# Optimization experiments

Measured on AMD Instinct MI355X. Metric: run time of the kernel, lower is better.

Reference implementation:

```python
import jax, jax.numpy as jnp
import numpy as np

NX, NY, NZ = 432, 496, 1
VX, VY, VZ = 0.16, 0.16, 4.0
XOFF = VX / 2 + 0.0
YOFF = VY / 2 + (-39.68)
ZOFF = VZ / 2 + (-3.0)
GRID = NZ * NX * NY
P, NPT, B = 100000, 32, 8
EPS = 1e-3


def setup_inputs() -> dict:
    key = jax.random.key(0)
    k1, k2, k3, k4 = jax.random.split(key, 4)
    voxels = jax.random.normal(k1, (P, NPT, 4), dtype=jnp.float32)
    num_points = jax.random.randint(k2, (P,), 1, NPT + 1, dtype=jnp.int32)
    b = jax.random.randint(k3, (P,), 0, B, dtype=jnp.int32)
    # unique BEV cells (17 coprime with GRID, P < GRID) -> deterministic scatter
    cell = (jnp.arange(P, dtype=jnp.int32) * 17) % GRID
    y = cell // NX
    x = cell % NX
    coords = jnp.stack([b, jnp.zeros_like(b), y, x], axis=1)  # [P,4] (b,z,y,x)
    W = jax.random.normal(k4, (64, 10), dtype=jnp.float32) * 0.1
    gamma = jnp.ones((64,), dtype=jnp.float32)
    beta = jnp.zeros((64,), dtype=jnp.float32)
    return {"voxels": voxels, "num_points": num_points, "coords": coords,
            "W": W, "gamma": gamma, "beta": beta}


def reference(voxels, num_points, coords, W, gamma, beta):
    cf = coords.astype(voxels.dtype)
    npf = num_points.astype(voxels.dtype)
    # cluster feature: offset from pillar mean
    points_mean = voxels[:, :, :3].sum(axis=1, keepdims=True) / npf[:, None, None]
    f_cluster = voxels[:, :, :3] - points_mean
    # center feature: offset from voxel center
    cx = cf[:, 3, None] * VX + XOFF
    cy = cf[:, 2, None] * VY + YOFF
    cz = cf[:, 1, None] * VZ + ZOFF
    f_center = jnp.stack([voxels[:, :, 0] - cx,
                          voxels[:, :, 1] - cy,
                          voxels[:, :, 2] - cz], axis=-1)
    feat = jnp.concatenate([voxels, f_cluster, f_center], axis=-1)  # [P,N,10]
    mask = (jnp.arange(NPT, dtype=jnp.int32)[None, :] < num_points[:, None])
    feat = feat * mask.astype(feat.dtype)[:, :, None]
    # linear(10->64, no bias) + BatchNorm1d (batch stats, biased var) + relu
    x = jnp.einsum('pnf,cf->pnc', feat, W)  # [P,N,64]
    mean = x.mean(axis=(0, 1))
    var = ((x - mean) ** 2).mean(axis=(0, 1))
    x = (x - mean) * jax.lax.rsqrt(var + EPS) * gamma + beta
    x = jax.nn.relu(x)
    pillars = x.max(axis=1)  # [P,64]
    idx = coords[:, 1] + coords[:, 2] * NX + coords[:, 3]
    bev = jnp.zeros((B, GRID, 64), dtype=pillars.dtype)
    bev = bev.at[coords[:, 0], idx].set(pillars)
    bev = jnp.transpose(bev, (0, 2, 1))  # [B,64,GRID]
    return bev.reshape(B, 64 * NZ, NY, NX)
```

## Files before the change

kernel.cpp:

```cpp
#include <hip/hip_runtime.h>

typedef unsigned short u16;

#define NXg 432
#define NYg 496
#define GRIDg (NXg*NYg)
#define NPTg 32
#define Bg 8
#define CHg 64
#define NSLOT 32

__device__ __forceinline__ float bf2f(u16 u){
    union { unsigned int i; float f; } x; x.i = ((unsigned int)u) << 16; return x.f;
}
__device__ __forceinline__ u16 f2bf(float f){
    union { float f; unsigned int i; } x; x.f = f;
    unsigned int i = x.i + 0x7FFFu + ((x.i >> 16) & 1u);
    return (u16)(i >> 16);
}
__device__ __forceinline__ bool is_bf16(const void* gamma){
    return ((*(const unsigned*)gamma) & 0xFFFFu) != 0u;
}

__global__ __launch_bounds__(256) void pfe_init(int* __restrict__ map, float* __restrict__ chsum,
                                                u16* __restrict__ pv, int P){
    int t = blockIdx.x*256 + threadIdx.x;
    ((int4*)map)[t] = make_int4(-1,-1,-1,-1);
    if (t < (NSLOT*128)/4) ((float4*)chsum)[t] = make_float4(0.f,0.f,0.f,0.f);
    if (t < 8) ((uint4*)(pv + (size_t)P*CHg))[t] = make_uint4(0u,0u,0u,0u);
}

__global__ __launch_bounds__(256) void pfe_pillar(
    const void* __restrict__ vox, const int* __restrict__ nump,
    const int* __restrict__ coords, const void* __restrict__ Wv,
    const void* __restrict__ gv,
    u16* __restrict__ pv, int* __restrict__ map, float* __restrict__ chsum,
    int P, int nwaves)
{
    __shared__ float4 pts[4][32];
    const bool isbf = is_bf16(gv);
    int lane = threadIdx.x & 63;
    int wid  = (blockIdx.x*256 + threadIdx.x) >> 6;
    int ws   = threadIdx.x >> 6;
    int n    = lane & 31;

    float w4,w5,w6,w7,w8,w9, wp0,wp1,wp2,wp3;
    bool gsel;
    {
        float w[10];
#pragma unroll
        for (int j=0;j<10;j++)
            w[j] = isbf ? bf2f(((const u16*)Wv)[lane*10 + j]) : ((const float*)Wv)[lane*10 + j];
        wp0 = w[0]+w[4]+w[7];
        wp1 = w[1]+w[5]+w[8];
        wp2 = w[2]+w[6]+w[9];
        wp3 = w[3];
        w4=w[4]; w5=w[5]; w6=w[6]; w7=w[7]; w8=w[8]; w9=w[9];
        float g = isbf ? bf2f(((const u16*)gv)[lane]) : ((const float*)gv)[lane];
        gsel = (g >= 0.f);
    }

    float sx = 0.f, sx2 = 0.f;

    for (int p = wid; p < P; p += nwaves) {
        int np = nump[p];
        int4 cc = *(const int4*)(coords + 4*p);
        float4 pt;
        if (isbf){
            ushort4 raw = *(const ushort4*)((const u16*)vox + ((size_t)p*NPTg + n)*4);
            pt = make_float4(bf2f(raw.x), bf2f(raw.y), bf2f(raw.z), bf2f(raw.w));
        } else {
            pt = *(const float4*)((const float*)vox + ((size_t)p*NPTg + n)*4);
        }
        if (lane < 32) pts[ws][n] = pt;

        float s0 = pt.x, s1 = pt.y, s2 = pt.z;
#pragma unroll
        for (int m = 1; m < 32; m <<= 1){
            s0 += __shfl_xor(s0, m, 64);
            s1 += __shfl_xor(s1, m, 64);
            s2 += __shfl_xor(s2, m, 64);
        }
        float inv = 1.0f / (float)np;
        float m0 = s0*inv, m1 = s1*inv, m2 = s2*inv;
        float ccx = (float)cc.w * 0.16f + 0.08f;
        float ccy = (float)cc.z * 0.16f + (0.08f - 39.68f);
        float ccz = (float)cc.y * 4.0f  + (2.0f - 3.0f);
        float d = -(m0*w4 + m1*w5 + m2*w6 + ccx*w7 + ccy*w8 + ccz*w9);

        const float4* row = pts[ws];
        float qmx = -3e38f, qmn = 3e38f, sq = 0.f, sq2 = 0.f;
        int k = 0;
        for (; k + 4 <= np; k += 4){
#pragma unroll
            for (int u = 0; u < 4; u++){
                float4 a = row[k+u];
                float q = fmaf(a.x, wp0, fmaf(a.y, wp1, fmaf(a.z, wp2, a.w*wp3)));
                qmx = fmaxf(qmx, q);
                qmn = fminf(qmn, q);
                sq += q;
                sq2 = fmaf(q, q, sq2);
            }
        }
        for (; k < np; k++){
            float4 a = row[k];
            float q = fmaf(a.x, wp0, fmaf(a.y, wp1, fmaf(a.z, wp2, a.w*wp3)));
            qmx = fmaxf(qmx, q);
            qmn = fminf(qmn, q);
            sq += q;
            sq2 = fmaf(q, q, sq2);
        }

        float npf = (float)np;
        sx  += sq + npf*d;
        sx2 += sq2 + d*(2.f*sq + npf*d);

        float fmx = qmx + d, fmn = qmn + d;
        if (np < NPTg){ fmx = fmaxf(fmx, 0.f); fmn = fminf(fmn, 0.f); }
        pv[(size_t)p*CHg + lane] = f2bf(gsel ? fmx : fmn);
        if (lane == 0) map[cc.x*GRIDg + cc.z*NXg + cc.w] = p;
    }

    float* slot = chsum + (blockIdx.x & (NSLOT-1))*128;
    atomicAdd(slot + lane, sx);
    atomicAdd(slot + 64 + lane, sx2);
}

__global__ __launch_bounds__(64) void pfe_stats(
    const float* __restrict__ chsum,
    const void* __restrict__ gv, const void* __restrict__ bv,
    float* __restrict__ sb, int P)
{
    const bool isbf = is_bf16(gv);
    int t = threadIdx.x;
    float S = 0.f, S2 = 0.f;
    for (int sl = 0; sl < NSLOT; sl++){
        S  += chsum[sl*128 + t];
        S2 += chsum[sl*128 + 64 + t];
    }
    float cnt = (float)P * (float)NPTg;
    float mean = S / cnt;
    float var  = S2 / cnt - mean*mean;
    float g  = isbf ? bf2f(((const u16*)gv)[t]) : ((const float*)gv)[t];
    float be = isbf ? bf2f(((const u16*)bv)[t]) : ((const float*)bv)[t];
    float sc = g * rsqrtf(var + 1e-3f);
    sb[t] = sc; sb[64 + t] = be - mean*sc;
}

__global__ __launch_bounds__(256) void pfe_postbn(
    u16* __restrict__ pv, const float* __restrict__ sb,
    const void* __restrict__ gv, int P)
{
    if (!is_bf16(gv)) return;
    int t = blockIdx.x*256 + threadIdx.x;
    if (t >= P*8) return;
    size_t i0 = (size_t)t*8;
    int c0 = (int)(i0 & 63);
    uint4 v = *(uint4*)(pv + i0);
    float4 sA = *(const float4*)(sb + c0);
    float4 sB = *(const float4*)(sb + c0 + 4);
    float4 bA = *(const float4*)(sb + 64 + c0);
    float4 bB = *(const float4*)(sb + 64 + c0 + 4);
#define PB(dw, slo, blo, shi, bhi) \
    ( (unsigned)f2bf(fmaxf(fmaf(slo, bf2f((u16)((dw) & 0xFFFFu)), blo), 0.f)) \
    | ((unsigned)f2bf(fmaxf(fmaf(shi, bf2f((u16)((dw) >> 16)),    bhi), 0.f)) << 16) )
    unsigned o0 = PB(v.x, sA.x, bA.x, sA.y, bA.y);
    unsigned o1 = PB(v.y, sA.z, bA.z, sA.w, bA.w);
    unsigned o2 = PB(v.z, sB.x, bB.x, sB.y, bB.y);
    unsigned o3 = PB(v.w, sB.z, bB.z, sB.w, bB.w);
#undef PB
    *(uint4*)(pv + i0) = make_uint4(o0, o1, o2, o3);
}

__global__ __launch_bounds__(192) void pfe_gather(
    const int* __restrict__ map, const u16* __restrict__ pv,
    const float* __restrict__ sb, const void* __restrict__ gv,
    void* __restrict__ out, int P)
{
    const bool isbf = is_bf16(gv);
    int b  = blockIdx.z;
    int c0 = blockIdx.y * 32;
    int px = blockIdx.x*768 + threadIdx.x*4;
    int4 m4 = *(const int4*)(map + (size_t)b*GRIDg + px);

    if (isbf){
        int p0 = (m4.x < 0) ? P : m4.x;
        int p1 = (m4.y < 0) ? P : m4.y;
        int p2 = (m4.z < 0) ? P : m4.z;
        int p3 = (m4.w < 0) ? P : m4.w;
        const uint4* r0 = (const uint4*)(pv + (size_t)p0*CHg + c0);
        const uint4* r1 = (const uint4*)(pv + (size_t)p1*CHg + c0);
        const uint4* r2 = (const uint4*)(pv + (size_t)p2*CHg + c0);
        const uint4* r3 = (const uint4*)(pv + (size_t)p3*CHg + c0);
        uint4 A0=r0[0], A1=r0[1], A2=r0[2], A3=r0[3];
        uint4 B0=r1[0], B1=r1[1], B2=r1[2], B3=r1[3];
        uint4 C0=r2[0], C1=r2[1], C2=r2[2], C3=r2[3];
        uint4 D0=r3[0], D1=r3[1], D2=r3[2], D3=r3[3];
        u16* ob = (u16*)out + ((size_t)(b*CHg + c0))*GRIDg + px;
#define GETB(Q0,Q1,Q2,Q3, COMP, CREL) { \
        unsigned w0=Q0.COMP, w1=Q1.COMP, w2=Q2.COMP, w3=Q3.COMP; \
        uint2 e, o; \
        e.x = __builtin_amdgcn_perm(w1, w0, 0x05040100u); \
        e.y = __builtin_amdgcn_perm(w3, w2, 0x05040100u); \
        o.x = __builtin_amdgcn_perm(w1, w0, 0x07060302u); \
        o.y = __builtin_amdgcn_perm(w3, w2, 0x07060302u); \
        *(uint2*)(ob + (size_t)(CREL)*GRIDg)     = e; \
        *(uint2*)(ob + (size_t)((CREL)+1)*GRIDg) = o; }
        GETB(A0,B0,C0,D0, x, 0)  GETB(A0,B0,C0,D0, y, 2)  GETB(A0,B0,C0,D0, z, 4)  GETB(A0,B0,C0,D0, w, 6)
        GETB(A1,B1,C1,D1, x, 8)  GETB(A1,B1,C1,D1, y, 10) GETB(A1,B1,C1,D1, z, 12) GETB(A1,B1,C1,D1, w, 14)
        GETB(A2,B2,C2,D2, x, 16) GETB(A2,B2,C2,D2, y, 18) GETB(A2,B2,C2,D2, z, 20) GETB(A2,B2,C2,D2, w, 22)
        GETB(A3,B3,C3,D3, x, 24) GETB(A3,B3,C3,D3, y, 26) GETB(A3,B3,C3,D3, z, 28) GETB(A3,B3,C3,D3, w, 30)
#undef GETB
    } else {
        bool v0 = m4.x >= 0, v1 = m4.y >= 0, v2 = m4.z >= 0, v3 = m4.w >= 0;
        int p0 = v0 ? m4.x : 0;
        int p1 = v1 ? m4.y : 0;
        int p2 = v2 ? m4.z : 0;
        int p3 = v3 ? m4.w : 0;
        const uint4* r0 = (const uint4*)(pv + (size_t)p0*CHg + c0);
        const uint4* r1 = (const uint4*)(pv + (size_t)p1*CHg + c0);
        const uint4* r2 = (const uint4*)(pv + (size_t)p2*CHg + c0);
        const uint4* r3 = (const uint4*)(pv + (size_t)p3*CHg + c0);
        uint4 A0=r0[0], A1=r0[1], A2=r0[2], A3=r0[3];
        uint4 B0=r1[0], B1=r1[1], B2=r1[2], B3=r1[3];
        uint4 C0=r2[0], C1=r2[1], C2=r2[2], C3=r2[3];
        uint4 D0=r3[0], D1=r3[1], D2=r3[2], D3=r3[3];
        float* obf = (float*)out + ((size_t)(b*CHg + c0))*GRIDg + px;
#define GETF(Q0,Q1,Q2,Q3, COMP, CREL) { \
        unsigned w0=Q0.COMP, w1=Q1.COMP, w2=Q2.COMP, w3=Q3.COMP; \
        float sce = sb[c0+(CREL)],   bie = sb[64+c0+(CREL)]; \
        float sco = sb[c0+(CREL)+1], bio = sb[64+c0+(CREL)+1]; \
        float4 oe, oo; \
        oe.x = v0 ? fmaxf(fmaf(sce, __uint_as_float(w0 << 16), bie), 0.f) : 0.f; \
        oe.y = v1 ? fmaxf(fmaf(sce, __uint_as_float(w1 << 16), bie), 0.f) : 0.f; \
        oe.z = v2 ? fmaxf(fmaf(sce, __uint_as_float(w2 << 16), bie), 0.f) : 0.f; \
        oe.w = v3 ? fmaxf(fmaf(sce, __uint_as_float(w3 << 16), bie), 0.f) : 0.f; \
        oo.x = v0 ? fmaxf(fmaf(sco, __uint_as_float(w0 & 0xFFFF0000u), bio), 0.f) : 0.f; \
        oo.y = v1 ? fmaxf(fmaf(sco, __uint_as_float(w1 & 0xFFFF0000u), bio), 0.f) : 0.f; \
        oo.z = v2 ? fmaxf(fmaf(sco, __uint_as_float(w2 & 0xFFFF0000u), bio), 0.f) : 0.f; \
        oo.w = v3 ? fmaxf(fmaf(sco, __uint_as_float(w3 & 0xFFFF0000u), bio), 0.f) : 0.f; \
        *(float4*)(obf + (size_t)(CREL)*GRIDg)     = oe; \
        *(float4*)(obf + (size_t)((CREL)+1)*GRIDg) = oo; }
        GETF(A0,B0,C0,D0, x, 0)  GETF(A0,B0,C0,D0, y, 2)  GETF(A0,B0,C0,D0, z, 4)  GETF(A0,B0,C0,D0, w, 6)
        GETF(A1,B1,C1,D1, x, 8)  GETF(A1,B1,C1,D1, y, 10) GETF(A1,B1,C1,D1, z, 12) GETF(A1,B1,C1,D1, w, 14)
        GETF(A2,B2,C2,D2, x, 16) GETF(A2,B2,C2,D2, y, 18) GETF(A2,B2,C2,D2, z, 20) GETF(A2,B2,C2,D2, w, 22)
        GETF(A3,B3,C3,D3, x, 24) GETF(A3,B3,C3,D3, y, 26) GETF(A3,B3,C3,D3, z, 28) GETF(A3,B3,C3,D3, w, 30)
#undef GETF
    }
}

extern "C" void kernel_launch(void* const* d_in, const int* in_sizes, int n_in,
                              void* d_out, int out_size, void* d_ws, size_t ws_size,
                              hipStream_t stream)
{
    const void* vox   = d_in[0];
    const int* nump   = (const int*)d_in[1];
    const int* coords = (const int*)d_in[2];
    const void* Wv    = d_in[3];
    const void* gv    = d_in[4];
    const void* bv    = d_in[5];
    int P = in_sizes[1];

    float* chsum = (float*)d_ws;
    float* sb    = (float*)((char*)d_ws + 16384);
    u16*   pv    = (u16*)((char*)d_ws + 32768);
    int*   map   = (int*)((char*)pv + (size_t)(P+1)*CHg*2);

    int initThreads = (Bg*GRIDg)/4;
    pfe_init<<<initThreads/256, 256, 0, stream>>>(map, chsum, pv, P);

    int blocks1 = 2048;
    pfe_pillar<<<blocks1, 256, 0, stream>>>(vox, nump, coords, Wv, gv, pv, map, chsum, P, blocks1*4);

    pfe_stats<<<1, 64, 0, stream>>>(chsum, gv, bv, sb, P);

    int pbBlocks = (P*8 + 255)/256;
    pfe_postbn<<<pbBlocks, 256, 0, stream>>>(pv, sb, gv, P);

    dim3 g3(GRIDg/768, 2, Bg);
    pfe_gather<<<g3, 192, 0, stream>>>(map, pv, sb, gv, d_out, P);
}
```

Baseline: 520.5 us.

## Fuse BN/ReLU into gather, drop postbn pass, nontemporal stores, global point reads

Removes the separate pfe_postbn kernel by applying the batch-norm scale/shift and ReLU inside the gather kernel for the bf16 path, with empty cells masked to zero instead of pointing at a zero sentinel row. Output stores become nontemporal to avoid polluting cache with the large BEV write. The pillar kernel stops staging points through LDS and reads each point row directly from global (wave-uniform broadcast loads), using readfirstlane for the wave index. The trade-off is more ALU work per output element in the gather and redundant global loads in the pillar loop.

```diff
diff --git a/kernel.cpp b/kernel.cpp
--- a/kernel.cpp
+++ b/kernel.cpp
@@ -1,6 +1,8 @@
 #include <hip/hip_runtime.h>
 
 typedef unsigned short u16;
+typedef unsigned uint2n __attribute__((ext_vector_type(2)));
+typedef float float4n __attribute__((ext_vector_type(4)));
 
 #define NXg 432
 #define NYg 496
@@ -22,12 +24,10 @@
     return ((*(const unsigned*)gamma) & 0xFFFFu) != 0u;
 }
 
-__global__ __launch_bounds__(256) void pfe_init(int* __restrict__ map, float* __restrict__ chsum,
-                                                u16* __restrict__ pv, int P){
+__global__ __launch_bounds__(256) void pfe_init(int* __restrict__ map, float* __restrict__ chsum){
     int t = blockIdx.x*256 + threadIdx.x;
     ((int4*)map)[t] = make_int4(-1,-1,-1,-1);
     if (t < (NSLOT*128)/4) ((float4*)chsum)[t] = make_float4(0.f,0.f,0.f,0.f);
-    if (t < 8) ((uint4*)(pv + (size_t)P*CHg))[t] = make_uint4(0u,0u,0u,0u);
 }
 
 __global__ __launch_bounds__(256) void pfe_pillar(
@@ -37,11 +37,10 @@
     u16* __restrict__ pv, int* __restrict__ map, float* __restrict__ chsum,
     int P, int nwaves)
 {
-    __shared__ float4 pts[4][32];
     const bool isbf = is_bf16(gv);
     int lane = threadIdx.x & 63;
-    int wid  = (blockIdx.x*256 + threadIdx.x) >> 6;
-    int ws   = threadIdx.x >> 6;
+    int wl   = __builtin_amdgcn_readfirstlane(threadIdx.x >> 6);
+    int wid  = blockIdx.x*4 + wl;
     int n    = lane & 31;
 
     float w4,w5,w6,w7,w8,w9, wp0,wp1,wp2,wp3;
@@ -65,6 +64,7 @@
     for (int p = wid; p < P; p += nwaves) {
         int np = nump[p];
         int4 cc = *(const int4*)(coords + 4*p);
+
         float4 pt;
         if (isbf){
             ushort4 raw = *(const ushort4*)((const u16*)vox + ((size_t)p*NPTg + n)*4);
@@ -72,8 +72,6 @@
         } else {
             pt = *(const float4*)((const float*)vox + ((size_t)p*NPTg + n)*4);
         }
-        if (lane < 32) pts[ws][n] = pt;
-
         float s0 = pt.x, s1 = pt.y, s2 = pt.z;
 #pragma unroll
         for (int m = 1; m < 32; m <<= 1){
@@ -88,28 +86,33 @@
         float ccz = (float)cc.y * 4.0f  + (2.0f - 3.0f);
         float d = -(m0*w4 + m1*w5 + m2*w6 + ccx*w7 + ccy*w8 + ccz*w9);
 
-        const float4* row = pts[ws];
         float qmx = -3e38f, qmn = 3e38f, sq = 0.f, sq2 = 0.f;
-        int k = 0;
-        for (; k + 4 <= np; k += 4){
-#pragma unroll
-            for (int u = 0; u < 4; u++){
-                float4 a = row[k+u];
-                float q = fmaf(a.x, wp0, fmaf(a.y, wp1, fmaf(a.z, wp2, a.w*wp3)));
-                qmx = fmaxf(qmx, q);
-                qmn = fminf(qmn, q);
-                sq += q;
-                sq2 = fmaf(q, q, sq2);
+#define PROC(ax,ay,az,aw) { \
+        float q = fmaf((ax), wp0, fmaf((ay), wp1, fmaf((az), wp2, (aw)*wp3))); \
+        qmx = fmaxf(qmx, q); qmn = fminf(qmn, q); \
+        sq += q; sq2 = fmaf(q, q, sq2); }
+        if (isbf){
+            const ushort4* rg = (const ushort4*)vox + (size_t)p*NPTg;
+            for (int k = 0; k < np; k++){
+                ushort4 r = rg[k];
+                PROC(bf2f(r.x), bf2f(r.y), bf2f(r.z), bf2f(r.w));
+            }
+        } else {
+            const float4* rg = (const float4*)vox + (size_t)p*NPTg;
+            int k = 0;
+            for (; k + 4 <= np; k += 4){
+                float4 a0 = rg[k+0], a1 = rg[k+1], a2 = rg[k+2], a3 = rg[k+3];
+                PROC(a0.x,a0.y,a0.z,a0.w);
+                PROC(a1.x,a1.y,a1.z,a1.w);
+                PROC(a2.x,a2.y,a2.z,a2.w);
+                PROC(a3.x,a3.y,a3.z,a3.w);
+            }
+            for (; k < np; k++){
+                float4 a = rg[k];
+                PROC(a.x,a.y,a.z,a.w);
             }
         }
-        for (; k < np; k++){
-            float4 a = row[k];
-            float q = fmaf(a.x, wp0, fmaf(a.y, wp1, fmaf(a.z, wp2, a.w*wp3)));
-            qmx = fmaxf(qmx, q);
-            qmn = fminf(qmn, q);
-            sq += q;
-            sq2 = fmaf(q, q, sq2);
-        }
+#undef PROC
 
         float npf = (float)np;
         sx  += sq + npf*d;
@@ -147,90 +150,63 @@
     sb[t] = sc; sb[64 + t] = be - mean*sc;
 }
 
-__global__ __launch_bounds__(256) void pfe_postbn(
-    u16* __restrict__ pv, const float* __restrict__ sb,
-    const void* __restrict__ gv, int P)
-{
-    if (!is_bf16(gv)) return;
-    int t = blockIdx.x*256 + threadIdx.x;
-    if (t >= P*8) return;
-    size_t i0 = (size_t)t*8;
-    int c0 = (int)(i0 & 63);
-    uint4 v = *(uint4*)(pv + i0);
-    float4 sA = *(const float4*)(sb + c0);
-    float4 sB = *(const float4*)(sb + c0 + 4);
-    float4 bA = *(const float4*)(sb + 64 + c0);
-    float4 bB = *(const float4*)(sb + 64 + c0 + 4);
-#define PB(dw, slo, blo, shi, bhi) \
-    ( (unsigned)f2bf(fmaxf(fmaf(slo, bf2f((u16)((dw) & 0xFFFFu)), blo), 0.f)) \
-    | ((unsigned)f2bf(fmaxf(fmaf(shi, bf2f((u16)((dw) >> 16)),    bhi), 0.f)) << 16) )
-    unsigned o0 = PB(v.x, sA.x, bA.x, sA.y, bA.y);
-    unsigned o1 = PB(v.y, sA.z, bA.z, sA.w, bA.w);
-    unsigned o2 = PB(v.z, sB.x, bB.x, sB.y, bB.y);
-    unsigned o3 = PB(v.w, sB.z, bB.z, sB.w, bB.w);
-#undef PB
-    *(uint4*)(pv + i0) = make_uint4(o0, o1, o2, o3);
-}
-
 __global__ __launch_bounds__(192) void pfe_gather(
     const int* __restrict__ map, const u16* __restrict__ pv,
     const float* __restrict__ sb, const void* __restrict__ gv,
-    void* __restrict__ out, int P)
+    void* __restrict__ out)
 {
     const bool isbf = is_bf16(gv);
     int b  = blockIdx.z;
     int c0 = blockIdx.y * 32;
     int px = blockIdx.x*768 + threadIdx.x*4;
     int4 m4 = *(const int4*)(map + (size_t)b*GRIDg + px);
+    bool v0 = m4.x >= 0, v1 = m4.y >= 0, v2 = m4.z >= 0, v3 = m4.w >= 0;
+    int p0 = v0 ? m4.x : 0;
+    int p1 = v1 ? m4.y : 0;
+    int p2 = v2 ? m4.z : 0;
+    int p3 = v3 ? m4.w : 0;
+    const uint4* r0 = (const uint4*)(pv + (size_t)p0*CHg + c0);
+    const uint4* r1 = (const uint4*)(pv + (size_t)p1*CHg + c0);
+    const uint4* r2 = (const uint4*)(pv + (size_t)p2*CHg + c0);
+    const uint4* r3 = (const uint4*)(pv + (size_t)p3*CHg + c0);
+    uint4 A0=r0[0], A1=r0[1], A2=r0[2], A3=r0[3];
+    uint4 B0=r1[0], B1=r1[1], B2=r1[2], B3=r1[3];
+    uint4 C0=r2[0], C1=r2[1], C2=r2[2], C3=r2[3];
+    uint4 D0=r3[0], D1=r3[1], D2=r3[2], D3=r3[3];
 
     if (isbf){
-        int p0 = (m4.x < 0) ? P : m4.x;
-        int p1 = (m4.y < 0) ? P : m4.y;
-        int p2 = (m4.z < 0) ? P : m4.z;
-        int p3 = (m4.w < 0) ? P : m4.w;
-        const uint4* r0 = (const uint4*)(pv + (size_t)p0*CHg + c0);
-        const uint4* r1 = (const uint4*)(pv + (size_t)p1*CHg + c0);
-        const uint4* r2 = (const uint4*)(pv + (size_t)p2*CHg + c0);
-        const uint4* r3 = (const uint4*)(pv + (size_t)p3*CHg + c0);
-        uint4 A0=r0[0], A1=r0[1], A2=r0[2], A3=r0[3];
-        uint4 B0=r1[0], B1=r1[1], B2=r1[2], B3=r1[3];
-        uint4 C0=r2[0], C1=r2[1], C2=r2[2], C3=r2[3];
-        uint4 D0=r3[0], D1=r3[1], D2=r3[2], D3=r3[3];
         u16* ob = (u16*)out + ((size_t)(b*CHg + c0))*GRIDg + px;
 #define GETB(Q0,Q1,Q2,Q3, COMP, CREL) { \
         unsigned w0=Q0.COMP, w1=Q1.COMP, w2=Q2.COMP, w3=Q3.COMP; \
-        uint2 e, o; \
-        e.x = __builtin_amdgcn_perm(w1, w0, 0x05040100u); \
-        e.y = __builtin_amdgcn_perm(w3, w2, 0x05040100u); \
-        o.x = __builtin_amdgcn_perm(w1, w0, 0x07060302u); \
-        o.y = __builtin_amdgcn_perm(w3, w2, 0x07060302u); \
-        *(uint2*)(ob + (size_t)(CREL)*GRIDg)     = e; \
-        *(uint2*)(ob + (size_t)((CREL)+1)*GRIDg) = o; }
+        float sce = sb[c0+(CREL)],   bie = sb[64+c0+(CREL)]; \
+        float sco = sb[c0+(CREL)+1], bio = sb[64+c0+(CREL)+1]; \
+        float e0 = v0 ? fmaxf(fmaf(sce, bf2f((u16)(w0 & 0xFFFFu)), bie), 0.f) : 0.f; \
+        float e1 = v1 ? fmaxf(fmaf(sce, bf2f((u16)(w1 & 0xFFFFu)), bie), 0.f) : 0.f; \
+        float e2 = v2 ? fmaxf(fmaf(sce, bf2f((u16)(w2 & 0xFFFFu)), bie), 0.f) : 0.f; \
+        float e3 = v3 ? fmaxf(fmaf(sce, bf2f((u16)(w3 & 0xFFFFu)), bie), 0.f) : 0.f; \
+        float o0 = v0 ? fmaxf(fmaf(sco, bf2f((u16)(w0 >> 16)), bio), 0.f) : 0.f; \
+        float o1 = v1 ? fmaxf(fmaf(sco, bf2f((u16)(w1 >> 16)), bio), 0.f) : 0.f; \
+        float o2 = v2 ? fmaxf(fmaf(sco, bf2f((u16)(w2 >> 16)), bio), 0.f) : 0.f; \
+        float o3 = v3 ? fmaxf(fmaf(sco, bf2f((u16)(w3 >> 16)), bio), 0.f) : 0.f; \
+        uint2n pe, po; \
+        pe.x = (unsigned)f2bf(e0) | ((unsigned)f2bf(e1) << 16); \
+        pe.y = (unsigned)f2bf(e2) | ((unsigned)f2bf(e3) << 16); \
+        po.x = (unsigned)f2bf(o0) | ((unsigned)f2bf(o1) << 16); \
+        po.y = (unsigned)f2bf(o2) | ((unsigned)f2bf(o3) << 16); \
+        __builtin_nontemporal_store(pe, (uint2n*)(ob + (size_t)(CREL)*GRIDg)); \
+        __builtin_nontemporal_store(po, (uint2n*)(ob + (size_t)((CREL)+1)*GRIDg)); }
         GETB(A0,B0,C0,D0, x, 0)  GETB(A0,B0,C0,D0, y, 2)  GETB(A0,B0,C0,D0, z, 4)  GETB(A0,B0,C0,D0, w, 6)
         GETB(A1,B1,C1,D1, x, 8)  GETB(A1,B1,C1,D1, y, 10) GETB(A1,B1,C1,D1, z, 12) GETB(A1,B1,C1,D1, w, 14)
         GETB(A2,B2,C2,D2, x, 16) GETB(A2,B2,C2,D2, y, 18) GETB(A2,B2,C2,D2, z, 20) GETB(A2,B2,C2,D2, w, 22)
         GETB(A3,B3,C3,D3, x, 24) GETB(A3,B3,C3,D3, y, 26) GETB(A3,B3,C3,D3, z, 28) GETB(A3,B3,C3,D3, w, 30)
 #undef GETB
     } else {
-        bool v0 = m4.x >= 0, v1 = m4.y >= 0, v2 = m4.z >= 0, v3 = m4.w >= 0;
-        int p0 = v0 ? m4.x : 0;
-        int p1 = v1 ? m4.y : 0;
-        int p2 = v2 ? m4.z : 0;
-        int p3 = v3 ? m4.w : 0;
-        const uint4* r0 = (const uint4*)(pv + (size_t)p0*CHg + c0);
-        const uint4* r1 = (const uint4*)(pv + (size_t)p1*CHg + c0);
-        const uint4* r2 = (const uint4*)(pv + (size_t)p2*CHg + c0);
-        const uint4* r3 = (const uint4*)(pv + (size_t)p3*CHg + c0);
-        uint4 A0=r0[0], A1=r0[1], A2=r0[2], A3=r0[3];
-        uint4 B0=r1[0], B1=r1[1], B2=r1[2], B3=r1[3];
-        uint4 C0=r2[0], C1=r2[1], C2=r2[2], C3=r2[3];
-        uint4 D0=r3[0], D1=r3[1], D2=r3[2], D3=r3[3];
         float* obf = (float*)out + ((size_t)(b*CHg + c0))*GRIDg + px;
 #define GETF(Q0,Q1,Q2,Q3, COMP, CREL) { \
         unsigned w0=Q0.COMP, w1=Q1.COMP, w2=Q2.COMP, w3=Q3.COMP; \
         float sce = sb[c0+(CREL)],   bie = sb[64+c0+(CREL)]; \
         float sco = sb[c0+(CREL)+1], bio = sb[64+c0+(CREL)+1]; \
-        float4 oe, oo; \
+        float4n oe, oo; \
         oe.x = v0 ? fmaxf(fmaf(sce, __uint_as_float(w0 << 16), bie), 0.f) : 0.f; \
         oe.y = v1 ? fmaxf(fmaf(sce, __uint_as_float(w1 << 16), bie), 0.f) : 0.f; \
         oe.z = v2 ? fmaxf(fmaf(sce, __uint_as_float(w2 << 16), bie), 0.f) : 0.f; \
@@ -239,8 +215,8 @@
         oo.y = v1 ? fmaxf(fmaf(sco, __uint_as_float(w1 & 0xFFFF0000u), bio), 0.f) : 0.f; \
         oo.z = v2 ? fmaxf(fmaf(sco, __uint_as_float(w2 & 0xFFFF0000u), bio), 0.f) : 0.f; \
         oo.w = v3 ? fmaxf(fmaf(sco, __uint_as_float(w3 & 0xFFFF0000u), bio), 0.f) : 0.f; \
-        *(float4*)(obf + (size_t)(CREL)*GRIDg)     = oe; \
-        *(float4*)(obf + (size_t)((CREL)+1)*GRIDg) = oo; }
+        __builtin_nontemporal_store(oe, (float4n*)(obf + (size_t)(CREL)*GRIDg)); \
+        __builtin_nontemporal_store(oo, (float4n*)(obf + (size_t)((CREL)+1)*GRIDg)); }
         GETF(A0,B0,C0,D0, x, 0)  GETF(A0,B0,C0,D0, y, 2)  GETF(A0,B0,C0,D0, z, 4)  GETF(A0,B0,C0,D0, w, 6)
         GETF(A1,B1,C1,D1, x, 8)  GETF(A1,B1,C1,D1, y, 10) GETF(A1,B1,C1,D1, z, 12) GETF(A1,B1,C1,D1, w, 14)
         GETF(A2,B2,C2,D2, x, 16) GETF(A2,B2,C2,D2, y, 18) GETF(A2,B2,C2,D2, z, 20) GETF(A2,B2,C2,D2, w, 22)
@@ -264,19 +240,16 @@
     float* chsum = (float*)d_ws;
     float* sb    = (float*)((char*)d_ws + 16384);
     u16*   pv    = (u16*)((char*)d_ws + 32768);
-    int*   map   = (int*)((char*)pv + (size_t)(P+1)*CHg*2);
+    int*   map   = (int*)((char*)pv + (size_t)P*CHg*2);
 
     int initThreads = (Bg*GRIDg)/4;
-    pfe_init<<<initThreads/256, 256, 0, stream>>>(map, chsum, pv, P);
+    pfe_init<<<initThreads/256, 256, 0, stream>>>(map, chsum);
 
     int blocks1 = 2048;
     pfe_pillar<<<blocks1, 256, 0, stream>>>(vox, nump, coords, Wv, gv, pv, map, chsum, P, blocks1*4);
 
     pfe_stats<<<1, 64, 0, stream>>>(chsum, gv, bv, sb, P);
 
-    int pbBlocks = (P*8 + 255)/256;
-    pfe_postbn<<<pbBlocks, 256, 0, stream>>>(pv, sb, gv, P);
-
     dim3 g3(GRIDg/768, 2, Bg);
-    pfe_gather<<<g3, 192, 0, stream>>>(map, pv, sb, gv, d_out, P);
-}
+    pfe_gather<<<g3, 192, 0, stream>>>(map, pv, sb, gv, d_out);
+}
```

New measurement: 514.8 us. Within noise of the previous version (-1.1%).
